# Performance work log

Measured on AMD Instinct MI355X. Metric: run time of the kernel, lower is better.

## Reference

```python
import jax, jax.numpy as jnp
import numpy as np
from jax import lax

DILATION_DEPTH = 10
N_REPEAT = 5
DILS = [2 ** i for i in range(DILATION_DEPTH)] * N_REPEAT  # 50 layers
N_RES, N_SKIP, N_FEAT = 32, 512, 8
B, T = 4, 16384


def _dconv(x, w, b, d):
    # valid (causal, no padding) dilated conv1d, kernel size 2: out[t] = w0*x[t] + w1*x[t+d]
    y = lax.conv_general_dilated(x, w, window_strides=(1,), padding='VALID',
                                 rhs_dilation=(d,), dimension_numbers=('NCH', 'OIH', 'NCH'))
    return y + b[None, :, None]


def _pw(x, w, b):
    # 1x1 conv as einsum; w: [out, in]
    return jnp.einsum('oc,bct->bot', w, x) + b[None, :, None]


def setup_inputs() -> dict:
    key = jax.random.key(0)
    ks = jax.random.split(key, 16)
    L = len(DILS)
    s = 0.1
    return {
        'input': jax.random.normal(ks[0], (B, T, N_FEAT), dtype=jnp.float32),
        'from_w': jax.random.normal(ks[1], (N_RES, N_FEAT, 1), dtype=jnp.float32) * s,
        'from_b': jax.random.normal(ks[2], (N_RES,), dtype=jnp.float32) * s,
        'sig_w': jax.random.normal(ks[3], (L, N_RES, N_RES, 2), dtype=jnp.float32) * s,
        'sig_b': jax.random.normal(ks[4], (L, N_RES), dtype=jnp.float32) * s,
        'tan_w': jax.random.normal(ks[5], (L, N_RES, N_RES, 2), dtype=jnp.float32) * s,
        'tan_b': jax.random.normal(ks[6], (L, N_RES), dtype=jnp.float32) * s,
        'skip_w': jax.random.normal(ks[7], (L, N_SKIP, N_RES, 1), dtype=jnp.float32) * s,
        'skip_b': jax.random.normal(ks[8], (L, N_SKIP), dtype=jnp.float32) * s,
        'res_w': jax.random.normal(ks[9], (L, N_RES, N_RES, 1), dtype=jnp.float32) * s,
        'res_b': jax.random.normal(ks[10], (L, N_RES), dtype=jnp.float32) * s,
        'post1_w': jax.random.normal(ks[11], (N_SKIP, N_SKIP, 1), dtype=jnp.float32) * s,
        'post1_b': jax.random.normal(ks[12], (N_SKIP,), dtype=jnp.float32) * s,
        'post2_w': jax.random.normal(ks[13], (1, N_SKIP, 1), dtype=jnp.float32) * s,
        'post2_b': jax.random.normal(ks[14], (1,), dtype=jnp.float32) * s,
    }


def reference(input, from_w, from_b, sig_w, sig_b, tan_w, tan_b,
              skip_w, skip_b, res_w, res_b, post1_w, post1_b, post2_w, post2_b):
    h = jnp.transpose(input, (0, 2, 1))                       # [B, F, T]
    h = _pw(h, from_w[:, :, 0], from_b)                       # [B, 32, T]
    Lout = h.shape[2] - sum(DILS)                             # final output length
    skip_sum = jnp.zeros((h.shape[0], N_SKIP, Lout), dtype=h.dtype)
    for i, d in enumerate(DILS):
        gate = jax.nn.sigmoid(_dconv(h, sig_w[i], sig_b[i], d)) * \
               jnp.tanh(_dconv(h, tan_w[i], tan_b[i], d))      # [B, 32, T_i - d]
        skip = _pw(gate, skip_w[i, :, :, 0], skip_b[i])        # [B, 512, T_i - d]
        skip_sum = skip_sum + skip[:, :, -Lout:]
        h = _pw(gate, res_w[i, :, :, 0], res_b[i]) + h[:, :, d:]
    o = jax.nn.elu(skip_sum)
    o = _pw(o, post1_w[:, :, 0], post1_b)
    o = jax.nn.elu(o)
    o = _pw(o, post2_w[:, :, 0], post2_b)                     # [B, 1, Lout]
    return o
```

## Files before the change

kernel.cpp:

```cpp
#include <hip/hip_runtime.h>
#include <hip/hip_bf16.h>

#define TLEN 16384
#define NB 4
#define NLAYER 50
#define SUMD 5115
#define LOUT 11269
#define K1 (NLAYER * 32)
#define MSKIP 512
#define FWOUT 256
#define FWIN 511
#define FP 36

typedef unsigned short u16;
typedef __attribute__((ext_vector_type(4))) float f32x4;
typedef __attribute__((ext_vector_type(8))) __bf16 bf16x8;

__device__ __forceinline__ u16 f2bf(float f) {
  __hip_bfloat16 h = __float2bfloat16(f);
  return *reinterpret_cast<u16*>(&h);
}
__device__ __forceinline__ float bf2f(u16 u) {
  __hip_bfloat16 h = *reinterpret_cast<__hip_bfloat16*>(&u);
  return __bfloat162float(h);
}

__global__ __launch_bounds__(256) void prep_k(
    const float* __restrict__ skip_w, const float* __restrict__ skip_b,
    const float* __restrict__ post1_w,
    const float* __restrict__ sig_w, const float* __restrict__ tan_w,
    const float* __restrict__ res_w,
    u16* __restrict__ Wskip, u16* __restrict__ P1, float* __restrict__ biasS,
    u16* __restrict__ WC, u16* __restrict__ RC) {
  int t = blockIdx.x * 256 + threadIdx.x;
  const int n1 = 512 * K1;
  const int n2 = n1 + 512 * 512;
  const int n3 = n2 + 512;
  const int n4 = n3 + NLAYER * 64 * 64;
  const int n5 = n4 + NLAYER * 32 * 32;
  if (t < n1) {
    int m = t / K1, k = t - m * K1;
    int i = k >> 5, c = k & 31;
    Wskip[t] = f2bf(skip_w[((size_t)i * 512 + m) * 32 + c]);
  } else if (t < n2) {
    int z = t - n1;
    P1[z] = f2bf(post1_w[z]);
  } else if (t < n3) {
    int c = t - n2;
    float s = 0.f;
    for (int i = 0; i < NLAYER; i++) s += skip_b[i * 512 + c];
    biasS[c] = s;
  } else if (t < n4) {
    int z = t - n3;
    int l = z >> 12, rem = z & 4095, o = rem >> 6, k = rem & 63;
    int c = k & 31, lr = k >> 5;
    float v;
    if (o < 32) v = sig_w[(((size_t)l * 32 + o) * 32 + c) * 2 + lr];
    else        v = tan_w[(((size_t)l * 32 + (o - 32)) * 32 + c) * 2 + lr];
    WC[z] = f2bf(v);
  } else if (t < n5) {
    int z = t - n4;
    int l = z >> 10, rem = z & 1023, o = rem >> 5, c = rem & 31;
    RC[z] = f2bf(res_w[((size_t)l * 32 + o) * 32 + c]);
  }
}

__global__ __launch_bounds__(256) void init_p(
    const float* __restrict__ inp, const float* __restrict__ fw,
    const float* __restrict__ fb, float* __restrict__ H, int t0, int cw) {
  __shared__ float FWs[256];
  __shared__ float FBs[32];
  int tid = threadIdx.x;
  FWs[tid] = fw[tid];
  if (tid < 32) FBs[tid] = fb[tid];
  __syncthreads();
  int gsz = gridDim.x * 256;
  int gid0 = blockIdx.x * 256 + tid;
  for (int b = 0; b < NB; b++) {
    const float* ib = inp + ((size_t)b * TLEN + t0) * 8;
    float* hb = H + (size_t)b * cw * 32;
    for (int p = gid0; p < cw; p += gsz) {
      float4 x0 = *reinterpret_cast<const float4*>(ib + (size_t)p * 8);
      float4 x1 = *reinterpret_cast<const float4*>(ib + (size_t)p * 8 + 4);
      float x[8] = {x0.x, x0.y, x0.z, x0.w, x1.x, x1.y, x1.z, x1.w};
      float* op = hb + (size_t)p * 32;
      #pragma unroll
      for (int r4 = 0; r4 < 8; r4++) {
        float4 o;
        #pragma unroll
        for (int j = 0; j < 4; j++) {
          int r = r4 * 4 + j;
          float acc = FBs[r];
          #pragma unroll
          for (int f = 0; f < 8; f++) acc += FWs[r * 8 + f] * x[f];
          ((float*)&o)[j] = acc;
        }
        *reinterpret_cast<float4*>(op + r4 * 4) = o;
      }
    }
  }
}

__global__ __launch_bounds__(512, 1) void fuse8_k(
    const float* __restrict__ src, float* __restrict__ dst,
    u16* __restrict__ G,
    const u16* __restrict__ WC, const u16* __restrict__ RC,
    const float* __restrict__ sb, const float* __restrict__ tb,
    const float* __restrict__ rb,
    int L0, int len_in, int cw, int clen) {
  __shared__ float HB[2][FWIN][FP];
  __shared__ u16 GT[8][16][40];
  int tid = threadIdx.x;
  int wv = tid >> 6, lane = tid & 63;
  int pc = lane & 15, kg = lane >> 4;
  int b = blockIdx.y;
  int len_out = len_in - 255;
  int pstart = cw - len_out + blockIdx.x * FWOUT;
  int g0 = pstart - 255;
  int wcount = (cw - g0 < FWIN) ? (cw - g0) : FWIN;
  int ocount = (cw - pstart < FWOUT) ? (cw - pstart) : FWOUT;

  const float* sp = src + ((size_t)b * cw + g0) * 32;
  for (int z = tid; z < wcount * 8; z += 512) {
    int lp = z >> 3, c4 = z & 7;
    *reinterpret_cast<float4*>(&HB[0][lp][c4 * 4]) =
        *reinterpret_cast<const float4*>(sp + (size_t)lp * 32 + c4 * 4);
  }
  __syncthreads();

  int cur = 0;
  for (int l = 0; l < 8; l++) {
    int d = 1 << l;
    int cumD = (2 << l) - 1;
    const u16* Wc = WC + (size_t)(L0 + l) * 4096;
    const u16* Rc = RC + (size_t)(L0 + l) * 1024;
    bf16x8 AW[4][2], AR[2];
    #pragma unroll
    for (int mt = 0; mt < 4; mt++) {
      AW[mt][0] = *reinterpret_cast<const bf16x8*>(Wc + (mt * 16 + pc) * 64 + kg * 8);
      AW[mt][1] = *reinterpret_cast<const bf16x8*>(Wc + (mt * 16 + pc) * 64 + 32 + kg * 8);
    }
    AR[0] = *reinterpret_cast<const bf16x8*>(Rc + pc * 32 + kg * 8);
    AR[1] = *reinterpret_cast<const bf16x8*>(Rc + (16 + pc) * 32 + kg * 8);
    float4 sbv0 = *reinterpret_cast<const float4*>(sb + (L0 + l) * 32 + kg * 4);
    float4 sbv1 = *reinterpret_cast<const float4*>(sb + (L0 + l) * 32 + 16 + kg * 4);
    float4 tbv0 = *reinterpret_cast<const float4*>(tb + (L0 + l) * 32 + kg * 4);
    float4 tbv1 = *reinterpret_cast<const float4*>(tb + (L0 + l) * 32 + 16 + kg * 4);
    float4 rbv0 = *reinterpret_cast<const float4*>(rb + (L0 + l) * 32 + kg * 4);
    float4 rbv1 = *reinterpret_cast<const float4*>(rb + (L0 + l) * 32 + 16 + kg * 4);

    int lo_local = wcount - cumD;
    int nit = (lo_local + 127) >> 7;
    for (int t = 0; t < nit; t++) {
      int lp = cumD + t * 128 + wv * 16 + pc;
      bool valid = lp < wcount;
      int lpc = valid ? lp : wcount - 1;

      float4 r0 = *reinterpret_cast<const float4*>(&HB[cur][lpc][kg * 8]);
      float4 r1 = *reinterpret_cast<const float4*>(&HB[cur][lpc][kg * 8 + 4]);
      float4 l0v = *reinterpret_cast<const float4*>(&HB[cur][lpc - d][kg * 8]);
      float4 l1v = *reinterpret_cast<const float4*>(&HB[cur][lpc - d][kg * 8 + 4]);

      union { u16 u[8]; bf16x8 v; } uL, uR;
      {
        float lf[8] = {l0v.x, l0v.y, l0v.z, l0v.w, l1v.x, l1v.y, l1v.z, l1v.w};
        float rf[8] = {r0.x, r0.y, r0.z, r0.w, r1.x, r1.y, r1.z, r1.w};
        #pragma unroll
        for (int j = 0; j < 8; j++) { uL.u[j] = f2bf(lf[j]); uR.u[j] = f2bf(rf[j]); }
      }

      f32x4 cs0 = {0.f, 0.f, 0.f, 0.f}, cs1 = {0.f, 0.f, 0.f, 0.f};
      f32x4 ct0 = {0.f, 0.f, 0.f, 0.f}, ct1 = {0.f, 0.f, 0.f, 0.f};
      cs0 = __builtin_amdgcn_mfma_f32_16x16x32_bf16(AW[0][0], uL.v, cs0, 0, 0, 0);
      cs0 = __builtin_amdgcn_mfma_f32_16x16x32_bf16(AW[0][1], uR.v, cs0, 0, 0, 0);
      cs1 = __builtin_amdgcn_mfma_f32_16x16x32_bf16(AW[1][0], uL.v, cs1, 0, 0, 0);
      cs1 = __builtin_amdgcn_mfma_f32_16x16x32_bf16(AW[1][1], uR.v, cs1, 0, 0, 0);
      ct0 = __builtin_amdgcn_mfma_f32_16x16x32_bf16(AW[2][0], uL.v, ct0, 0, 0, 0);
      ct0 = __builtin_amdgcn_mfma_f32_16x16x32_bf16(AW[2][1], uR.v, ct0, 0, 0, 0);
      ct1 = __builtin_amdgcn_mfma_f32_16x16x32_bf16(AW[3][0], uL.v, ct1, 0, 0, 0);
      ct1 = __builtin_amdgcn_mfma_f32_16x16x32_bf16(AW[3][1], uR.v, ct1, 0, 0, 0);

      u16 gs0[4], gs1[4];
      {
        float sa[4] = {sbv0.x, sbv0.y, sbv0.z, sbv0.w};
        float sbq[4] = {sbv1.x, sbv1.y, sbv1.z, sbv1.w};
        float ta[4] = {tbv0.x, tbv0.y, tbv0.z, tbv0.w};
        float tbq[4] = {tbv1.x, tbv1.y, tbv1.z, tbv1.w};
        #pragma unroll
        for (int r = 0; r < 4; r++) {
          float s0 = cs0[r] + sa[r], t0v = ct0[r] + ta[r];
          float s1 = cs1[r] + sbq[r], t1v = ct1[r] + tbq[r];
          float g0v = (1.f / (1.f + __expf(-s0))) * (2.f / (1.f + __expf(-2.f * t0v)) - 1.f);
          float g1v = (1.f / (1.f + __expf(-s1))) * (2.f / (1.f + __expf(-2.f * t1v)) - 1.f);
          gs0[r] = f2bf(g0v);
          gs1[r] = f2bf(g1v);
        }
      }
      uint2 pk0 = {(unsigned)gs0[0] | ((unsigned)gs0[1] << 16),
                   (unsigned)gs0[2] | ((unsigned)gs0[3] << 16)};
      uint2 pk1 = {(unsigned)gs1[0] | ((unsigned)gs1[1] << 16),
                   (unsigned)gs1[2] | ((unsigned)gs1[3] << 16)};
      *reinterpret_cast<uint2*>(&GT[wv][pc][kg * 4]) = pk0;
      *reinterpret_cast<uint2*>(&GT[wv][pc][16 + kg * 4]) = pk1;

      int p = g0 + lpc;
      if (valid && p >= pstart && p < pstart + ocount && p >= cw - clen) {
        int n = b * clen + (p - (cw - clen));
        u16* gr = G + (size_t)n * K1 + (L0 + l) * 32;
        *reinterpret_cast<uint2*>(gr + kg * 4) = pk0;
        *reinterpret_cast<uint2*>(gr + 16 + kg * 4) = pk1;
      }

      bf16x8 bg = *reinterpret_cast<const bf16x8*>(&GT[wv][pc][kg * 8]);
      float4 ha = *reinterpret_cast<const float4*>(&HB[cur][lpc][kg * 4]);
      float4 hb2 = *reinterpret_cast<const float4*>(&HB[cur][lpc][16 + kg * 4]);
      f32x4 h0 = {ha.x + rbv0.x, ha.y + rbv0.y, ha.z + rbv0.z, ha.w + rbv0.w};
      f32x4 h1 = {hb2.x + rbv1.x, hb2.y + rbv1.y, hb2.z + rbv1.z, hb2.w + rbv1.w};
      f32x4 d0 = __builtin_amdgcn_mfma_f32_16x16x32_bf16(AR[0], bg, h0, 0, 0, 0);
      f32x4 d1 = __builtin_amdgcn_mfma_f32_16x16x32_bf16(AR[1], bg, h1, 0, 0, 0);
      if (valid) {
        *reinterpret_cast<float4*>(&HB[cur ^ 1][lp][kg * 4]) = float4{d0[0], d0[1], d0[2], d0[3]};
        *reinterpret_cast<float4*>(&HB[cur ^ 1][lp][16 + kg * 4]) = float4{d1[0], d1[1], d1[2], d1[3]};
      }
    }
    __syncthreads();
    cur ^= 1;
  }

  float* dp = dst + ((size_t)b * cw + pstart) * 32;
  for (int z = tid; z < ocount * 8; z += 512) {
    int lp = z >> 3, c4 = z & 7;
    *reinterpret_cast<float4*>(dp + (size_t)lp * 32 + c4 * 4) =
        *reinterpret_cast<float4*>(&HB[cur][255 + lp][c4 * 4]);
  }
}

__global__ __launch_bounds__(256, 2) void layer_p(
    const float* __restrict__ src, float* __restrict__ dst,
    u16* __restrict__ G,
    const u16* __restrict__ Wc, const u16* __restrict__ Rc,
    const float* __restrict__ sbl, const float* __restrict__ tbl,
    const float* __restrict__ rbl,
    int layer, int d, int lo, int cw, int clen) {
  __shared__ u16 GT[4][16][40];
  __shared__ float HRT[4][16][36];
  int tid = threadIdx.x;
  int wv = tid >> 6, lane = tid & 63;
  int pc = lane & 15, kg = lane >> 4;
  int b = blockIdx.y;

  bf16x8 AW[4][2], AR[2];
  #pragma unroll
  for (int mt = 0; mt < 4; mt++) {
    AW[mt][0] = *reinterpret_cast<const bf16x8*>(Wc + (mt * 16 + pc) * 64 + kg * 8);
    AW[mt][1] = *reinterpret_cast<const bf16x8*>(Wc + (mt * 16 + pc) * 64 + 32 + kg * 8);
  }
  AR[0] = *reinterpret_cast<const bf16x8*>(Rc + pc * 32 + kg * 8);
  AR[1] = *reinterpret_cast<const bf16x8*>(Rc + (16 + pc) * 32 + kg * 8);

  float4 sbv0 = *reinterpret_cast<const float4*>(sbl + kg * 4);
  float4 sbv1 = *reinterpret_cast<const float4*>(sbl + 16 + kg * 4);
  float4 tbv0 = *reinterpret_cast<const float4*>(tbl + kg * 4);
  float4 tbv1 = *reinterpret_cast<const float4*>(tbl + 16 + kg * 4);
  float4 rbv0 = *reinterpret_cast<const float4*>(rbl + kg * 4);
  float4 rbv1 = *reinterpret_cast<const float4*>(rbl + 16 + kg * 4);

  int idx = blockIdx.x * 64 + wv * 16 + pc;
  bool valid = idx < lo;
  int idc = valid ? idx : lo - 1;
  int p = cw - lo + idc;

  const float* hp = src + ((size_t)b * cw + p) * 32 + kg * 8;
  float4 r0 = *reinterpret_cast<const float4*>(hp);
  float4 r1 = *reinterpret_cast<const float4*>(hp + 4);
  const float* hq = hp - (size_t)d * 32;
  float4 l0 = *reinterpret_cast<const float4*>(hq);
  float4 l1 = *reinterpret_cast<const float4*>(hq + 4);

  union { u16 u[8]; bf16x8 v; } uL, uR;
  {
    float lf[8] = {l0.x, l0.y, l0.z, l0.w, l1.x, l1.y, l1.z, l1.w};
    float rf[8] = {r0.x, r0.y, r0.z, r0.w, r1.x, r1.y, r1.z, r1.w};
    #pragma unroll
    for (int j = 0; j < 8; j++) { uL.u[j] = f2bf(lf[j]); uR.u[j] = f2bf(rf[j]); }
  }
  *reinterpret_cast<float4*>(&HRT[wv][pc][kg * 8]) = r0;
  *reinterpret_cast<float4*>(&HRT[wv][pc][kg * 8 + 4]) = r1;

  f32x4 cs0 = {0.f, 0.f, 0.f, 0.f}, cs1 = {0.f, 0.f, 0.f, 0.f};
  f32x4 ct0 = {0.f, 0.f, 0.f, 0.f}, ct1 = {0.f, 0.f, 0.f, 0.f};
  cs0 = __builtin_amdgcn_mfma_f32_16x16x32_bf16(AW[0][0], uL.v, cs0, 0, 0, 0);
  cs0 = __builtin_amdgcn_mfma_f32_16x16x32_bf16(AW[0][1], uR.v, cs0, 0, 0, 0);
  cs1 = __builtin_amdgcn_mfma_f32_16x16x32_bf16(AW[1][0], uL.v, cs1, 0, 0, 0);
  cs1 = __builtin_amdgcn_mfma_f32_16x16x32_bf16(AW[1][1], uR.v, cs1, 0, 0, 0);
  ct0 = __builtin_amdgcn_mfma_f32_16x16x32_bf16(AW[2][0], uL.v, ct0, 0, 0, 0);
  ct0 = __builtin_amdgcn_mfma_f32_16x16x32_bf16(AW[2][1], uR.v, ct0, 0, 0, 0);
  ct1 = __builtin_amdgcn_mfma_f32_16x16x32_bf16(AW[3][0], uL.v, ct1, 0, 0, 0);
  ct1 = __builtin_amdgcn_mfma_f32_16x16x32_bf16(AW[3][1], uR.v, ct1, 0, 0, 0);

  u16 gs0[4], gs1[4];
  {
    float sa[4] = {sbv0.x, sbv0.y, sbv0.z, sbv0.w};
    float sbq[4] = {sbv1.x, sbv1.y, sbv1.z, sbv1.w};
    float ta[4] = {tbv0.x, tbv0.y, tbv0.z, tbv0.w};
    float tbq[4] = {tbv1.x, tbv1.y, tbv1.z, tbv1.w};
    #pragma unroll
    for (int r = 0; r < 4; r++) {
      float s0 = cs0[r] + sa[r], t0v = ct0[r] + ta[r];
      float s1 = cs1[r] + sbq[r], t1v = ct1[r] + tbq[r];
      float g0 = (1.f / (1.f + __expf(-s0))) * (2.f / (1.f + __expf(-2.f * t0v)) - 1.f);
      float g1 = (1.f / (1.f + __expf(-s1))) * (2.f / (1.f + __expf(-2.f * t1v)) - 1.f);
      gs0[r] = f2bf(g0);
      gs1[r] = f2bf(g1);
    }
  }
  uint2 pk0 = {(unsigned)gs0[0] | ((unsigned)gs0[1] << 16),
               (unsigned)gs0[2] | ((unsigned)gs0[3] << 16)};
  uint2 pk1 = {(unsigned)gs1[0] | ((unsigned)gs1[1] << 16),
               (unsigned)gs1[2] | ((unsigned)gs1[3] << 16)};
  *reinterpret_cast<uint2*>(&GT[wv][pc][kg * 4]) = pk0;
  *reinterpret_cast<uint2*>(&GT[wv][pc][16 + kg * 4]) = pk1;

  if (valid && p >= cw - clen) {
    int n = b * clen + (p - (cw - clen));
    u16* gr = G + (size_t)n * K1 + layer * 32;
    *reinterpret_cast<uint2*>(gr + kg * 4) = pk0;
    *reinterpret_cast<uint2*>(gr + 16 + kg * 4) = pk1;
  }

  bf16x8 bg = *reinterpret_cast<const bf16x8*>(&GT[wv][pc][kg * 8]);
  float4 ha = *reinterpret_cast<const float4*>(&HRT[wv][pc][kg * 4]);
  float4 hbq = *reinterpret_cast<const float4*>(&HRT[wv][pc][16 + kg * 4]);
  f32x4 h0 = {ha.x + rbv0.x, ha.y + rbv0.y, ha.z + rbv0.z, ha.w + rbv0.w};
  f32x4 h1 = {hbq.x + rbv1.x, hbq.y + rbv1.y, hbq.z + rbv1.z, hbq.w + rbv1.w};
  f32x4 d0 = __builtin_amdgcn_mfma_f32_16x16x32_bf16(AR[0], bg, h0, 0, 0, 0);
  f32x4 d1 = __builtin_amdgcn_mfma_f32_16x16x32_bf16(AR[1], bg, h1, 0, 0, 0);
  if (valid) {
    float* dp = dst + ((size_t)b * cw + p) * 32;
    *reinterpret_cast<float4*>(dp + kg * 4) = float4{d0[0], d0[1], d0[2], d0[3]};
    *reinterpret_cast<float4*>(dp + 16 + kg * 4) = float4{d1[0], d1[1], d1[2], d1[3]};
  }
}

__global__ __launch_bounds__(256) void gemm_k(
    const u16* __restrict__ A, const u16* __restrict__ B,
    const float* __restrict__ bias, u16* __restrict__ Out,
    const float* __restrict__ w2, const float* __restrict__ b2p,
    float* __restrict__ outv,
    int N, int K, int FIN, int clen, int t0f) {
  __shared__ __align__(16) u16 As[128 * 32];
  __shared__ __align__(16) u16 Bs[128 * 32];
  int tid = threadIdx.x;

  int nwg = gridDim.x;
  int orig = blockIdx.x;
  int q = nwg >> 3, r8 = nwg & 7, xcd = orig & 7, sl = orig >> 3;
  int wg = (xcd < r8 ? xcd * (q + 1) : r8 * (q + 1) + (xcd - r8) * q) + sl;
  int m0 = (wg & 3) * 128;
  int n0 = (wg >> 2) * 128;

  int lane = tid & 63, wv = tid >> 6;
  int wm = wv >> 1, wn = wv & 1;
  int row16 = lane & 15, kg = lane >> 4;
  int l3 = lane & 3, lr = lane >> 2;

  f32x4 acc[4][4];
  #pragma unroll
  for (int i = 0; i < 4; i++)
    #pragma unroll
    for (int j = 0; j < 4; j++) acc[i][j] = f32x4{0.f, 0.f, 0.f, 0.f};

  for (int k0 = 0; k0 < K; k0 += 32) {
    #pragma unroll
    for (int i = 0; i < 2; i++) {
      int c = wv * 2 + i;
      int row = c * 16 + lr;
      const u16* ga = A + (size_t)(m0 + row) * K + k0 + l3 * 8;
      __builtin_amdgcn_global_load_lds(
          (const __attribute__((address_space(1))) void*)ga,
          (__attribute__((address_space(3))) void*)(As + c * 512), 16, 0, 0);
      int nr = n0 + row;
      if (nr > N - 1) nr = N - 1;
      const u16* gb = B + (size_t)nr * K + k0 + l3 * 8;
      __builtin_amdgcn_global_load_lds(
          (const __attribute__((address_space(1))) void*)gb,
          (__attribute__((address_space(3))) void*)(Bs + c * 512), 16, 0, 0);
    }
    __syncthreads();

    bf16x8 af[4], bfr[4];
    #pragma unroll
    for (int mf = 0; mf < 4; mf++)
      af[mf] = *reinterpret_cast<const bf16x8*>(&As[(wm * 64 + mf * 16 + row16) * 32 + kg * 8]);
    #pragma unroll
    for (int nf = 0; nf < 4; nf++)
      bfr[nf] = *reinterpret_cast<const bf16x8*>(&Bs[(wn * 64 + nf * 16 + row16) * 32 + kg * 8]);
    #pragma unroll
    for (int mf = 0; mf < 4; mf++)
      #pragma unroll
      for (int nf = 0; nf < 4; nf++)
        acc[mf][nf] = __builtin_amdgcn_mfma_f32_16x16x32_bf16(af[mf], bfr[nf], acc[mf][nf], 0, 0, 0);
    __syncthreads();
  }

  if (!FIN) {
    #pragma unroll
    for (int mf = 0; mf < 4; mf++) {
      int rowb = m0 + wm * 64 + mf * 16 + kg * 4;
      float b0 = bias[rowb], b1 = bias[rowb + 1], b2 = bias[rowb + 2], b3 = bias[rowb + 3];
      #pragma unroll
      for (int nf = 0; nf < 4; nf++) {
        int col = n0 + wn * 64 + nf * 16 + row16;
        if (col < N) {
          float v0 = acc[mf][nf][0] + b0, v1 = acc[mf][nf][1] + b1;
          float v2 = acc[mf][nf][2] + b2, v3 = acc[mf][nf][3] + b3;
          v0 = v0 > 0.f ? v0 : expm1f(v0);
          v1 = v1 > 0.f ? v1 : expm1f(v1);
          v2 = v2 > 0.f ? v2 : expm1f(v2);
          v3 = v3 > 0.f ? v3 : expm1f(v3);
          uint2 pk = {(unsigned)f2bf(v0) | ((unsigned)f2bf(v1) << 16),
                      (unsigned)f2bf(v2) | ((unsigned)f2bf(v3) << 16)};
          *reinterpret_cast<uint2*>(Out + (size_t)col * 512 + rowb) = pk;
        }
      }
    }
  } else {
    float part[4] = {0.f, 0.f, 0.f, 0.f};
    #pragma unroll
    for (int mf = 0; mf < 4; mf++) {
      int rowb = m0 + wm * 64 + mf * 16 + kg * 4;
      float b0 = bias[rowb], b1 = bias[rowb + 1], b2 = bias[rowb + 2], b3 = bias[rowb + 3];
      float w0 = w2[rowb], w1 = w2[rowb + 1], w2v = w2[rowb + 2], w3 = w2[rowb + 3];
      #pragma unroll
      for (int nf = 0; nf < 4; nf++) {
        float v0 = acc[mf][nf][0] + b0, v1 = acc[mf][nf][1] + b1;
        float v2 = acc[mf][nf][2] + b2, v3 = acc[mf][nf][3] + b3;
        v0 = v0 > 0.f ? v0 : expm1f(v0);
        v1 = v1 > 0.f ? v1 : expm1f(v1);
        v2 = v2 > 0.f ? v2 : expm1f(v2);
        v3 = v3 > 0.f ? v3 : expm1f(v3);
        part[nf] += w0 * v0 + w1 * v1 + w2v * v2 + w3 * v3;
      }
    }
    #pragma unroll
    for (int nf = 0; nf < 4; nf++) {
      float p = part[nf];
      p += __shfl_xor(p, 16);
      p += __shfl_xor(p, 32);
      if (kg == 0) {
        int col = n0 + wn * 64 + nf * 16 + row16;
        if (col < N) {
          if (m0 == 0 && wm == 0) p += b2p[0];
          int bb = col / clen, tc = col - bb * clen;
          atomicAdd(outv + (size_t)bb * LOUT + t0f + tc, p);
        }
      }
    }
  }
}

extern "C" void kernel_launch(void* const* d_in, const int* in_sizes, int n_in,
                              void* d_out, int out_size, void* d_ws, size_t ws_size,
                              hipStream_t stream) {
  const float* input   = (const float*)d_in[0];
  const float* from_w  = (const float*)d_in[1];
  const float* from_b  = (const float*)d_in[2];
  const float* sig_w   = (const float*)d_in[3];
  const float* sig_b   = (const float*)d_in[4];
  const float* tan_w   = (const float*)d_in[5];
  const float* tan_b   = (const float*)d_in[6];
  const float* skip_w  = (const float*)d_in[7];
  const float* skip_b  = (const float*)d_in[8];
  const float* res_w   = (const float*)d_in[9];
  const float* res_b   = (const float*)d_in[10];
  const float* post1_w = (const float*)d_in[11];
  const float* post1_b = (const float*)d_in[12];
  const float* post2_w = (const float*)d_in[13];
  const float* post2_b = (const float*)d_in[14];

  auto al = [](size_t x) { return (x + 255) & ~(size_t)255; };
  size_t oW  = 0;
  size_t oP1 = oW  + al((size_t)512 * K1 * 2);
  size_t oB  = oP1 + al((size_t)512 * 512 * 2);
  size_t oWC = oB  + al((size_t)512 * 4);
  size_t oRC = oWC + al((size_t)NLAYER * 64 * 64 * 2);
  size_t wend = oRC + al((size_t)NLAYER * 32 * 32 * 2);

  int NC = 32, CL = 0;
  size_t oH0 = wend, oH1 = wend, oG = wend, oE = wend;
  const int cand[6] = {1, 2, 4, 8, 16, 32};
  for (int ci = 0; ci < 6; ci++) {
    int nc = cand[ci];
    int cl = (LOUT + nc - 1) / nc;
    int cw = cl + SUMD;
    size_t hB = al((size_t)NB * 32 * cw * 4);
    size_t gB = al((size_t)NB * cl * K1 * 2);
    size_t eB = al((size_t)512 * NB * cl * 2);
    size_t need = wend + 2 * hB + gB + eB;
    if (need <= ws_size || nc == 32) {
      NC = nc; CL = cl;
      oH0 = wend; oH1 = oH0 + hB; oG = oH1 + hB; oE = oG + gB;
      break;
    }
  }

  char* ws = (char*)d_ws;
  u16*   Wskip = (u16*)(ws + oW);
  u16*   P1    = (u16*)(ws + oP1);
  float* biasS = (float*)(ws + oB);
  u16*   WC    = (u16*)(ws + oWC);
  u16*   RC    = (u16*)(ws + oRC);
  float* H0    = (float*)(ws + oH0);
  float* H1    = (float*)(ws + oH1);
  u16*   G     = (u16*)(ws + oG);
  u16*   E     = (u16*)(ws + oE);

  hipMemsetAsync(d_out, 0, (size_t)out_size * sizeof(float), stream);

  int prep_items = 512 * K1 + 512 * 512 + 512 + NLAYER * 64 * 64 + NLAYER * 32 * 32;
  prep_k<<<(prep_items + 255) / 256, 256, 0, stream>>>(
      skip_w, skip_b, post1_w, sig_w, tan_w, res_w, Wskip, P1, biasS, WC, RC);

  for (int c = 0; c < NC; c++) {
    int t0 = c * CL;
    if (t0 >= LOUT) break;
    int clen = LOUT - t0 < CL ? LOUT - t0 : CL;
    int cw = clen + SUMD;

    init_p<<<256, 256, 0, stream>>>(input, from_w, from_b, H0, t0, cw);

    float* a = H0;
    float* b2 = H1;
    int len = cw;
    for (int cyc = 0; cyc < 5; cyc++) {
      int L0 = cyc * 10;
      int lo8 = len - 255;
      int tiles = (lo8 + FWOUT - 1) / FWOUT;
      fuse8_k<<<dim3(tiles, NB), 512, 0, stream>>>(
          a, b2, G, WC, RC, sig_b, tan_b, res_b, L0, len, cw, clen);
      { float* t = a; a = b2; b2 = t; }
      len = lo8;
      for (int j = 0; j < 2; j++) {
        int li = L0 + 8 + j, d = 256 << j;
        int lo = len - d;
        layer_p<<<dim3((lo + 63) / 64, NB), 256, 0, stream>>>(
            a, b2, G, WC + (size_t)li * 4096, RC + (size_t)li * 1024,
            sig_b + li * 32, tan_b + li * 32, res_b + li * 32,
            li, d, lo, cw, clen);
        { float* t = a; a = b2; b2 = t; }
        len = lo;
      }
    }

    int Nc = NB * clen;
    int ntile = (Nc + 127) / 128;
    gemm_k<<<4 * ntile, 256, 0, stream>>>(Wskip, G, biasS, E,
                                          post2_w, post2_b, (float*)d_out,
                                          Nc, K1, 0, clen, t0);
    gemm_k<<<4 * ntile, 256, 0, stream>>>(P1, E, post1_b, E,
                                          post2_w, post2_b, (float*)d_out,
                                          Nc, 512, 1, clen, t0);
  }
}
```

Baseline: 728.7 us.

## Double fuse8 block to 1024 threads and restage gemm tiles with K=64

The fused 8-layer kernel now runs 1024 threads (16 waves) per block, so each pass covers 256 positions instead of 128. Its LDS row padding shrinks from 36 to 34 floats so the doubled gate buffer still fits in LDS. That padding leaves rows only 8-byte aligned while the kernel still does float4 LDS reads and writes, which risks misaligned or split accesses. The skip GEMM drops global_load_lds in favour of register-staged 128-bit loads into padded [128][72] tiles, processes K=64 per barrier, and zero-fills out-of-range B rows, aiming to halve barriers and reduce LDS bank conflicts.

Measured after the change: 741.6 us. Within noise of the previous version (+1.8%).

```diff
diff --git a/kernel.cpp b/kernel.cpp
--- a/kernel.cpp
+++ b/kernel.cpp
@@ -10,7 +10,7 @@
 #define MSKIP 512
 #define FWOUT 256
 #define FWIN 511
-#define FP 36
+#define FP 34
 
 typedef unsigned short u16;
 typedef __attribute__((ext_vector_type(4))) float f32x4;
@@ -101,7 +101,7 @@
   }
 }
 
-__global__ __launch_bounds__(512, 1) void fuse8_k(
+__global__ __launch_bounds__(1024, 1) void fuse8_k(
     const float* __restrict__ src, float* __restrict__ dst,
     u16* __restrict__ G,
     const u16* __restrict__ WC, const u16* __restrict__ RC,
@@ -109,7 +109,7 @@
     const float* __restrict__ rb,
     int L0, int len_in, int cw, int clen) {
   __shared__ float HB[2][FWIN][FP];
-  __shared__ u16 GT[8][16][40];
+  __shared__ u16 GT[16][16][40];
   int tid = threadIdx.x;
   int wv = tid >> 6, lane = tid & 63;
   int pc = lane & 15, kg = lane >> 4;
@@ -121,7 +121,7 @@
   int ocount = (cw - pstart < FWOUT) ? (cw - pstart) : FWOUT;
 
   const float* sp = src + ((size_t)b * cw + g0) * 32;
-  for (int z = tid; z < wcount * 8; z += 512) {
+  for (int z = tid; z < wcount * 8; z += 1024) {
     int lp = z >> 3, c4 = z & 7;
     *reinterpret_cast<float4*>(&HB[0][lp][c4 * 4]) =
         *reinterpret_cast<const float4*>(sp + (size_t)lp * 32 + c4 * 4);
@@ -150,9 +150,9 @@
     float4 rbv1 = *reinterpret_cast<const float4*>(rb + (L0 + l) * 32 + 16 + kg * 4);
 
     int lo_local = wcount - cumD;
-    int nit = (lo_local + 127) >> 7;
+    int nit = (lo_local + 255) >> 8;
     for (int t = 0; t < nit; t++) {
-      int lp = cumD + t * 128 + wv * 16 + pc;
+      int lp = cumD + t * 256 + wv * 16 + pc;
       bool valid = lp < wcount;
       int lpc = valid ? lp : wcount - 1;
 
@@ -228,7 +228,7 @@
   }
 
   float* dp = dst + ((size_t)b * cw + pstart) * 32;
-  for (int z = tid; z < ocount * 8; z += 512) {
+  for (int z = tid; z < ocount * 8; z += 1024) {
     int lp = z >> 3, c4 = z & 7;
     *reinterpret_cast<float4*>(dp + (size_t)lp * 32 + c4 * 4) =
         *reinterpret_cast<float4*>(&HB[cur][255 + lp][c4 * 4]);
@@ -348,8 +348,8 @@
     const float* __restrict__ w2, const float* __restrict__ b2p,
     float* __restrict__ outv,
     int N, int K, int FIN, int clen, int t0f) {
-  __shared__ __align__(16) u16 As[128 * 32];
-  __shared__ __align__(16) u16 Bs[128 * 32];
+  __shared__ u16 As[128][72];
+  __shared__ u16 Bs[128][72];
   int tid = threadIdx.x;
 
   int nwg = gridDim.x;
@@ -362,7 +362,6 @@
   int lane = tid & 63, wv = tid >> 6;
   int wm = wv >> 1, wn = wv & 1;
   int row16 = lane & 15, kg = lane >> 4;
-  int l3 = lane & 3, lr = lane >> 2;
 
   f32x4 acc[4][4];
   #pragma unroll
@@ -370,36 +369,45 @@
     #pragma unroll
     for (int j = 0; j < 4; j++) acc[i][j] = f32x4{0.f, 0.f, 0.f, 0.f};
 
-  for (int k0 = 0; k0 < K; k0 += 32) {
-    #pragma unroll
-    for (int i = 0; i < 2; i++) {
-      int c = wv * 2 + i;
-      int row = c * 16 + lr;
-      const u16* ga = A + (size_t)(m0 + row) * K + k0 + l3 * 8;
-      __builtin_amdgcn_global_load_lds(
-          (const __attribute__((address_space(1))) void*)ga,
-          (__attribute__((address_space(3))) void*)(As + c * 512), 16, 0, 0);
-      int nr = n0 + row;
-      if (nr > N - 1) nr = N - 1;
-      const u16* gb = B + (size_t)nr * K + k0 + l3 * 8;
-      __builtin_amdgcn_global_load_lds(
-          (const __attribute__((address_space(1))) void*)gb,
-          (__attribute__((address_space(3))) void*)(Bs + c * 512), 16, 0, 0);
+  int rS = tid >> 1, qS = tid & 1;
+  for (int k0 = 0; k0 < K; k0 += 64) {
+    {
+      const uint4* asrc = reinterpret_cast<const uint4*>(A + (size_t)(m0 + rS) * K + k0 + qS * 32);
+      uint4 a0 = asrc[0], a1 = asrc[1], a2 = asrc[2], a3 = asrc[3];
+      *reinterpret_cast<uint4*>(&As[rS][qS * 32]) = a0;
+      *reinterpret_cast<uint4*>(&As[rS][qS * 32 + 8]) = a1;
+      *reinterpret_cast<uint4*>(&As[rS][qS * 32 + 16]) = a2;
+      *reinterpret_cast<uint4*>(&As[rS][qS * 32 + 24]) = a3;
+    }
+    {
+      int nr = n0 + rS;
+      uint4 b0 = {0,0,0,0}, b1 = {0,0,0,0}, b2 = {0,0,0,0}, b3 = {0,0,0,0};
+      if (nr < N) {
+        const uint4* bsrc = reinterpret_cast<const uint4*>(B + (size_t)nr * K + k0 + qS * 32);
+        b0 = bsrc[0]; b1 = bsrc[1]; b2 = bsrc[2]; b3 = bsrc[3];
+      }
+      *reinterpret_cast<uint4*>(&Bs[rS][qS * 32]) = b0;
+      *reinterpret_cast<uint4*>(&Bs[rS][qS * 32 + 8]) = b1;
+      *reinterpret_cast<uint4*>(&Bs[rS][qS * 32 + 16]) = b2;
+      *reinterpret_cast<uint4*>(&Bs[rS][qS * 32 + 24]) = b3;
     }
     __syncthreads();
 
-    bf16x8 af[4], bfr[4];
-    #pragma unroll
-    for (int mf = 0; mf < 4; mf++)
-      af[mf] = *reinterpret_cast<const bf16x8*>(&As[(wm * 64 + mf * 16 + row16) * 32 + kg * 8]);
-    #pragma unroll
-    for (int nf = 0; nf < 4; nf++)
-      bfr[nf] = *reinterpret_cast<const bf16x8*>(&Bs[(wn * 64 + nf * 16 + row16) * 32 + kg * 8]);
-    #pragma unroll
-    for (int mf = 0; mf < 4; mf++)
+    #pragma unroll
+    for (int s = 0; s < 2; s++) {
+      bf16x8 af[4], bfr[4];
+      #pragma unroll
+      for (int mf = 0; mf < 4; mf++)
+        af[mf] = *reinterpret_cast<const bf16x8*>(&As[wm * 64 + mf * 16 + row16][s * 32 + kg * 8]);
       #pragma unroll
       for (int nf = 0; nf < 4; nf++)
-        acc[mf][nf] = __builtin_amdgcn_mfma_f32_16x16x32_bf16(af[mf], bfr[nf], acc[mf][nf], 0, 0, 0);
+        bfr[nf] = *reinterpret_cast<const bf16x8*>(&Bs[wn * 64 + nf * 16 + row16][s * 32 + kg * 8]);
+      #pragma unroll
+      for (int mf = 0; mf < 4; mf++)
+        #pragma unroll
+        for (int nf = 0; nf < 4; nf++)
+          acc[mf][nf] = __builtin_amdgcn_mfma_f32_16x16x32_bf16(af[mf], bfr[nf], acc[mf][nf], 0, 0, 0);
+    }
     __syncthreads();
   }
 
@@ -536,7 +544,7 @@
       int L0 = cyc * 10;
       int lo8 = len - 255;
       int tiles = (lo8 + FWOUT - 1) / FWOUT;
-      fuse8_k<<<dim3(tiles, NB), 512, 0, stream>>>(
+      fuse8_k<<<dim3(tiles, NB), 1024, 0, stream>>>(
           a, b2, G, WC, RC, sig_b, tan_b, res_b, L0, len, cw, clen);
       { float* t = a; a = b2; b2 = t; }
       len = lo8;
```
